# Kernel optimization log

Hardware: AMD Instinct MI355X
Metric: run time of the kernel (lower is better)

## Reference

```python
import jax, jax.numpy as jnp
import numpy as np

B, V, M, H = 256, 128, 256, 1024
TIMING_DIM = 10          # ceil(log2(max_timesteps=1024))
DECAY_ALPHA = 0.99
IN_DIM = (V + TIMING_DIM + 1 + 1) * M  # 35840


def setup_inputs() -> dict:
    key = jax.random.key(0)
    ks = jax.random.split(key, 12)
    x = jax.random.uniform(ks[0], (B, V), dtype=jnp.float32)
    memory = jax.random.uniform(ks[1], (B, M, V), dtype=jnp.float32)
    memory_timings = jax.random.randint(ks[2], (B, M), 0, 1000).astype(jnp.int64)
    memory_surprise = jax.random.uniform(ks[3], (B, M), dtype=jnp.float32)
    last_prediction = jax.random.uniform(ks[4], (B, V), dtype=jnp.float32)
    s1 = 1.0 / np.sqrt(IN_DIM)
    s2 = 1.0 / np.sqrt(H)
    W1 = jax.random.uniform(ks[5], (IN_DIM, H), dtype=jnp.float32, minval=-s1, maxval=s1)
    b1 = jnp.zeros((H,), jnp.float32)
    Wg = jax.random.uniform(ks[6], (IN_DIM, H), dtype=jnp.float32, minval=-s1, maxval=s1)
    bg = jnp.zeros((H,), jnp.float32)
    W2 = jax.random.uniform(ks[7], (H, V), dtype=jnp.float32, minval=-s2, maxval=s2)
    b2 = jnp.zeros((V,), jnp.float32)
    return {"x": x, "memory": memory, "memory_timings": memory_timings,
            "memory_surprise": memory_surprise, "last_prediction": last_prediction,
            "W1": W1, "b1": b1, "Wg": Wg, "bg": bg, "W2": W2, "b2": b2}


def _step(x, memory, memory_timings, memory_surprise, last_prediction):
    # surprise of incoming token under last prediction
    surprise = -jnp.log(jnp.sum(x * last_prediction, axis=1) + 1e-8)  # [B]
    # age + decay
    timings = memory_timings + 1
    surp = memory_surprise * DECAY_ALPHA
    # ring-buffer roll, write newest at slot 0
    mem = jnp.roll(memory, 1, axis=1).at[:, 0, :].set(x)
    timings = jnp.roll(timings, 1, axis=1).at[:, 0].set(0)
    surp = jnp.roll(surp, 1, axis=1).at[:, 0].set(surprise)
    # sort by age ascending, gather memory/surprise
    idx = jnp.argsort(timings, axis=1)                               # [B,M]
    sorted_timings = jnp.take_along_axis(timings, idx, axis=1)       # [B,M]
    sorted_memory = jnp.take_along_axis(mem, idx[..., None], axis=1)  # [B,M,V]
    sorted_surprise = jnp.take_along_axis(surp, idx, axis=1)          # [B,M]
    # binary encode timings
    powers = 2 ** jnp.arange(TIMING_DIM, dtype=sorted_timings.dtype)
    bits = ((sorted_timings[..., None] // powers) % 2).astype(jnp.float32)  # [B,M,T]
    norm_t = sorted_timings.astype(jnp.float32) / (
        jnp.max(sorted_timings, axis=1, keepdims=True).astype(jnp.float32) + 1.0)
    pred_input = jnp.concatenate(
        [sorted_memory.reshape(B, -1), bits.reshape(B, -1),
         norm_t.reshape(B, -1), sorted_surprise.reshape(B, -1)], axis=1)  # [B, IN_DIM]
    return pred_input


def reference(x, memory, memory_timings, memory_surprise, last_prediction,
              W1, b1, Wg, bg, W2, b2):
    pred_input = _step(x, memory, memory_timings, memory_surprise, last_prediction)
    # gated dense network: h = (xW1+b1) * sigmoid(xWg+bg); logits = hW2+b2
    h = (pred_input @ W1 + b1) * jax.nn.sigmoid(pred_input @ Wg + bg)
    return h @ W2 + b2
```

## Files before the change

### kernel.cpp

```cpp
#include <hip/hip_runtime.h>
#include <stdint.h>
#include <math.h>

#define BB 256
#define VV 128
#define MM 256
#define TDIM 10
#define HH 1024
#define IN_DIM 35840
#define KSPLIT 16
#define KSLICE 2240
#define BK 32
#define NCHUNK 70

using f32x4  = __attribute__((ext_vector_type(4))) float;
using bf16x8 = __attribute__((ext_vector_type(8))) short;

__device__ __forceinline__ unsigned short f2bf(float f) {
    unsigned int u = __float_as_uint(f);
    unsigned int r = (u + 0x7FFFu + ((u >> 16) & 1u)) >> 16;
    return (unsigned short)r;
}

__device__ __forceinline__ void gload_lds16(const void* g, void* l) {
    __builtin_amdgcn_global_load_lds(
        (const __attribute__((address_space(1))) unsigned int*)g,
        (__attribute__((address_space(3))) unsigned int*)l,
        16, 0, 0);
}

__global__ __launch_bounds__(512)
void k_build(const float* __restrict__ x, const float* __restrict__ memory,
             const int* __restrict__ timings, const float* __restrict__ msurp,
             const float* __restrict__ lastp, short* __restrict__ A)
{
    int b = blockIdx.x, t = threadIdx.x;
    __shared__ int t_s[MM], idx_s[MM], st_s[MM];
    __shared__ float s_surprise;

    if (t < MM) t_s[t] = (t == 0) ? 0 : timings[b*MM + t - 1] + 1;
    if (t < 64) {
        float v = x[b*VV + t] * lastp[b*VV + t]
                + x[b*VV + t + 64] * lastp[b*VV + t + 64];
        #pragma unroll
        for (int off = 32; off > 0; off >>= 1)
            v += __shfl_down(v, off, 64);
        if (t == 0) s_surprise = -logf(v + 1e-8f);
    }
    __syncthreads();

    if (t < MM) {
        int ti = t_s[t], cnt = 0;
        #pragma unroll 4
        for (int j = 0; j < MM; ++j) {
            int tj = t_s[j];
            cnt += (tj < ti) || (tj == ti && j < t);
        }
        idx_s[cnt] = t;
        st_s[cnt]  = ti;
    }
    __syncthreads();

    short* Ab = A + (size_t)b * IN_DIM;
    if (t < MM) {
        float invm = 1.f / ((float)st_s[MM-1] + 1.f);
        int st = st_s[t], src = idx_s[t];
        #pragma unroll
        for (int tt = 0; tt < TDIM; ++tt)
            Ab[32768 + t*TDIM + tt] = (short)f2bf((float)((st >> tt) & 1));
        Ab[35328 + t] = (short)f2bf((float)st * invm);
        float sv = (src == 0) ? s_surprise : msurp[b*MM + src - 1] * 0.99f;
        Ab[35584 + t] = (short)f2bf(sv);
    }

    int q4 = t >> 7, v = t & (VV-1);
    float xv = x[b*VV + v];
    #pragma unroll 8
    for (int p = q4; p < MM; p += 4) {
        int src = idx_s[p];
        int row = (src == 0) ? 0 : src - 1;
        float mv = memory[((size_t)b*MM + row)*VV + v];
        float val = (src == 0) ? xv : mv;
        Ab[p*VV + v] = (short)f2bf(val);
    }
}

__global__ __launch_bounds__(512, 4)
void k_gemm(const short* __restrict__ A, const float* __restrict__ W1,
            const float* __restrict__ Wg, float* __restrict__ P)
{
    int ks = blockIdx.x;
    int xt = blockIdx.y;
    const float* W = (xt < 16) ? W1 : Wg;
    int wcol0 = (xt & 15) * 64;
    int pcol0 = xt * 64;
    int k0 = ks * KSLICE;

    __shared__ bf16x8 As8[3][1024];
    __shared__ float  Wl[3][2048];

    int t = threadIdx.x;
    int l = t & 63, wv = t >> 6;
    int r = l & 15, q = l >> 4;
    int wm = wv & 3, nh = wv >> 2;

    int aoff[4];
    #pragma unroll
    for (int mt = 0; mt < 4; ++mt) {
        int R = wm*64 + mt*16 + r;
        aoff[mt] = R*4 + (q ^ ((R >> 1) & 3));
    }
    int ncol[2];
    #pragma unroll
    for (int nt = 0; nt < 2; ++nt) {
        int n = nh*32 + nt*16 + r;
        ncol[nt] = n ^ (q << 4);
    }

    f32x4 acc[4][2];
    #pragma unroll
    for (int mt = 0; mt < 4; ++mt)
        #pragma unroll
        for (int nt = 0; nt < 2; ++nt)
            acc[mt][nt] = (f32x4){0.f, 0.f, 0.f, 0.f};

    int wkk = t >> 4;
    int wnF = ((t & 15) * 4) ^ (((wkk >> 3) & 3) << 4);

#define STAGE(sbuf, cc) do {                                                  \
        int kc_ = k0 + (cc)*BK;                                               \
        {   int G_ = t;                                                       \
            int m_ = G_ >> 2;                                                 \
            int kb_ = (G_ & 3) ^ ((m_ >> 1) & 3);                             \
            gload_lds16(A + (size_t)m_*IN_DIM + kc_ + kb_*8,                  \
                        (char*)&As8[sbuf][0] + (size_t)(t & ~63)*16);         \
        }                                                                     \
        {   int G_ = t + 512;                                                 \
            int m_ = G_ >> 2;                                                 \
            int kb_ = (G_ & 3) ^ ((m_ >> 1) & 3);                             \
            gload_lds16(A + (size_t)m_*IN_DIM + kc_ + kb_*8,                  \
                        (char*)&As8[sbuf][0] + (size_t)((t & ~63) + 512)*16); \
        }                                                                     \
        gload_lds16(W + (size_t)(kc_ + wkk)*HH + wcol0 + wnF,                 \
                    (char*)&Wl[sbuf][0] + (size_t)(t & ~63)*16);              \
    } while (0)

    STAGE(0, 0);
    STAGE(1, 1);
    STAGE(2, 2);
    asm volatile("s_waitcnt vmcnt(6)" ::: "memory");
    __builtin_amdgcn_s_barrier();

    for (int c = 0; c < NCHUNK; ++c) {
        int buf = c % 3;

        bf16x8 af[4], bfr[2];
        #pragma unroll
        for (int mt = 0; mt < 4; ++mt) af[mt] = As8[buf][aoff[mt]];
        #pragma unroll
        for (int nt = 0; nt < 2; ++nt) {
            const float* wb = &Wl[buf][ncol[nt]];
            bf16x8 bb;
            #pragma unroll
            for (int j = 0; j < 8; ++j)
                bb[j] = (short)f2bf(wb[(q*8 + j)*64]);
            bfr[nt] = bb;
        }
        #pragma unroll
        for (int mt = 0; mt < 4; ++mt)
            #pragma unroll
            for (int nt = 0; nt < 2; ++nt)
                acc[mt][nt] = __builtin_amdgcn_mfma_f32_16x16x32_bf16(
                    af[mt], bfr[nt], acc[mt][nt], 0, 0, 0);

        __builtin_amdgcn_s_barrier();
        {
            int cn = (c + 3 < NCHUNK) ? c + 3 : NCHUNK - 1;
            STAGE(buf, cn);
        }
        asm volatile("s_waitcnt vmcnt(6)" ::: "memory");
        __builtin_amdgcn_s_barrier();
    }
#undef STAGE

    #pragma unroll
    for (int mt = 0; mt < 4; ++mt)
        #pragma unroll
        for (int nt = 0; nt < 2; ++nt)
            #pragma unroll
            for (int rg = 0; rg < 4; ++rg) {
                int m = wm*64 + mt*16 + q*4 + rg;
                int n = pcol0 + nh*32 + nt*16 + r;
                P[((size_t)ks*BB + m)*2048 + n] = acc[mt][nt][rg];
            }
}

__global__ __launch_bounds__(512)
void k_tail(const float* __restrict__ P, const float* __restrict__ b1,
            const float* __restrict__ bg, const float* __restrict__ W2,
            const float* __restrict__ b2, float* __restrict__ out)
{
    int b = blockIdx.x, t = threadIdx.x;
    __shared__ f32x4 part[512];
    __shared__ float hs[HH];
    __shared__ float s2[512];

    const f32x4* P4 = (const f32x4*)P;
    f32x4 s = (f32x4){0.f, 0.f, 0.f, 0.f};
    #pragma unroll
    for (int ks = 0; ks < KSPLIT; ++ks)
        s += P4[((size_t)ks*BB + b)*512 + t];
    part[t] = s;
    __syncthreads();

    if (t < 256) {
        f32x4 p1 = part[t]       + ((const f32x4*)b1)[t];
        f32x4 pg = part[t + 256] + ((const f32x4*)bg)[t];
        f32x4 o;
        #pragma unroll
        for (int j = 0; j < 4; ++j)
            o[j] = p1[j] / (1.f + expf(-pg[j]));
        ((f32x4*)hs)[t] = o;
    }
    __syncthreads();

    int v = t & 127, kh = t >> 7;
    const float* wp = W2 + (size_t)kh*256*VV + v;
    const float* hk = hs + kh*256;
    float acc = 0.f;
    #pragma unroll 8
    for (int k = 0; k < 256; ++k)
        acc += hk[k] * wp[(size_t)k*VV];
    s2[t] = acc;
    __syncthreads();
    if (t < 128)
        out[(size_t)b*VV + v] = s2[t] + s2[t+128] + s2[t+256] + s2[t+384] + b2[v];
}

extern "C" void kernel_launch(void* const* d_in, const int* in_sizes, int n_in,
                              void* d_out, int out_size, void* d_ws, size_t ws_size,
                              hipStream_t stream)
{
    const float* x    = (const float*)d_in[0];
    const float* mem  = (const float*)d_in[1];
    const int*   tim  = (const int*)d_in[2];
    const float* msur = (const float*)d_in[3];
    const float* lp   = (const float*)d_in[4];
    const float* W1   = (const float*)d_in[5];
    const float* b1   = (const float*)d_in[6];
    const float* Wg   = (const float*)d_in[7];
    const float* bg   = (const float*)d_in[8];
    const float* W2   = (const float*)d_in[9];
    const float* b2   = (const float*)d_in[10];
    float* out = (float*)d_out;

    short* A = (short*)d_ws;
    float* P = (float*)((char*)d_ws + 18350080);

    k_build <<<256, 512, 0, stream>>>(x, mem, tim, msur, lp, A);
    k_gemm  <<<dim3(KSPLIT, 32), 512, 0, stream>>>(A, W1, Wg, P);
    k_tail  <<<256, 512, 0, stream>>>(P, b1, bg, W2, b2, out);
}
```

Measured before the change: 403.0 us.

## Load A fragments directly to registers and convert W to bf16 once in LDS

The GEMM no longer stages A and fp32 W tiles into LDS with a triple buffer. Each wave now loads its own A rows straight from global memory into MFMA fragment registers, prefetched one chunk ahead. W is read into registers two chunks ahead, converted to bf16 once per element, and written into a small double-buffered swizzled LDS tile. The goal is to cut LDS footprint and traffic and remove redundant per-wave fp32-to-bf16 conversion. The cost is uncoalesced-ish direct global A loads and more register pressure, with a different 32x64 per-wave tiling.

```diff
diff --git a/kernel.cpp b/kernel.cpp
--- a/kernel.cpp
+++ b/kernel.cpp
@@ -22,13 +22,6 @@
     return (unsigned short)r;
 }
 
-__device__ __forceinline__ void gload_lds16(const void* g, void* l) {
-    __builtin_amdgcn_global_load_lds(
-        (const __attribute__((address_space(1))) unsigned int*)g,
-        (__attribute__((address_space(3))) unsigned int*)l,
-        16, 0, 0);
-}
-
 __global__ __launch_bounds__(512)
 void k_build(const float* __restrict__ x, const float* __restrict__ memory,
              const int* __restrict__ timings, const float* __restrict__ msurp,
@@ -96,101 +89,109 @@
     int pcol0 = xt * 64;
     int k0 = ks * KSLICE;
 
-    __shared__ bf16x8 As8[3][1024];
-    __shared__ float  Wl[3][2048];
+    __shared__ bf16x8 Ws8[2][256];
 
     int t = threadIdx.x;
     int l = t & 63, wv = t >> 6;
     int r = l & 15, q = l >> 4;
-    int wm = wv & 3, nh = wv >> 2;
-
-    int aoff[4];
-    #pragma unroll
-    for (int mt = 0; mt < 4; ++mt) {
-        int R = wm*64 + mt*16 + r;
-        aoff[mt] = R*4 + (q ^ ((R >> 1) & 3));
-    }
-    int ncol[2];
-    #pragma unroll
-    for (int nt = 0; nt < 2; ++nt) {
-        int n = nh*32 + nt*16 + r;
-        ncol[nt] = n ^ (q << 4);
-    }
-
-    f32x4 acc[4][2];
-    #pragma unroll
-    for (int mt = 0; mt < 4; ++mt)
-        #pragma unroll
-        for (int nt = 0; nt < 2; ++nt)
+
+    const short* arow[2];
+    #pragma unroll
+    for (int mt = 0; mt < 2; ++mt) {
+        int R = wv*32 + mt*16 + r;
+        arow[mt] = A + (size_t)R*IN_DIM + k0 + q*8;
+    }
+
+    int boff[4];
+    #pragma unroll
+    for (int nt = 0; nt < 4; ++nt) {
+        int R = nt*16 + r;
+        boff[nt] = R*4 + (q ^ ((R >> 1) & 3));
+    }
+
+    f32x4 acc[2][4];
+    #pragma unroll
+    for (int mt = 0; mt < 2; ++mt)
+        #pragma unroll
+        for (int nt = 0; nt < 4; ++nt)
             acc[mt][nt] = (f32x4){0.f, 0.f, 0.f, 0.f};
 
-    int wkk = t >> 4;
-    int wnF = ((t & 15) * 4) ^ (((wkk >> 3) & 3) << 4);
-
-#define STAGE(sbuf, cc) do {                                                  \
-        int kc_ = k0 + (cc)*BK;                                               \
-        {   int G_ = t;                                                       \
-            int m_ = G_ >> 2;                                                 \
-            int kb_ = (G_ & 3) ^ ((m_ >> 1) & 3);                             \
-            gload_lds16(A + (size_t)m_*IN_DIM + kc_ + kb_*8,                  \
-                        (char*)&As8[sbuf][0] + (size_t)(t & ~63)*16);         \
+    int wn = l;
+    int wkg = wv >> 1, whalf = wv & 1;
+    int wslot16 = (wn*4 + (wkg ^ ((wn >> 1) & 3))) * 16 + whalf * 8;
+    const float* wbase = W + (size_t)(k0 + wv*4)*HH + wcol0 + wn;
+
+#define LOADA(AF, cc) do {                                                    \
+        int ko_ = (cc)*BK;                                                    \
+        _Pragma("unroll")                                                     \
+        for (int mt_ = 0; mt_ < 2; ++mt_)                                     \
+            AF[mt_] = *(const bf16x8*)(arow[mt_] + ko_);                      \
+    } while (0)
+
+#define WLOAD(wreg, cc) do {                                                  \
+        const float* wp_ = wbase + (size_t)(cc)*BK*HH;                        \
+        _Pragma("unroll")                                                     \
+        for (int j_ = 0; j_ < 4; ++j_) wreg[j_] = wp_[(size_t)j_*HH];         \
+    } while (0)
+
+#define WCONV(wreg, wdst) do {                                                \
+        unsigned int lo_ = (unsigned int)f2bf(wreg[0])                        \
+                         | ((unsigned int)f2bf(wreg[1]) << 16);               \
+        unsigned int hi_ = (unsigned int)f2bf(wreg[2])                        \
+                         | ((unsigned int)f2bf(wreg[3]) << 16);               \
+        unsigned int* d_ = (unsigned int*)((char*)&Ws8[wdst][0] + wslot16);   \
+        d_[0] = lo_; d_[1] = hi_;                                             \
+    } while (0)
+
+    bf16x8 afA[2], afB[2];
+    float wA[4], wB[4], w0[4];
+
+    WLOAD(w0, 0);
+    LOADA(afA, 0);
+    WLOAD(wA, 1);
+    WCONV(w0, 0);
+    asm volatile("s_waitcnt lgkmcnt(0)" ::: "memory");
+    __builtin_amdgcn_s_barrier();
+
+#define CHUNK(c, AF, AFN, WCUR, WNXT) do {                                    \
+        int cA_ = ((c) + 1 < NCHUNK) ? (c) + 1 : NCHUNK - 1;                  \
+        int cW_ = ((c) + 2 < NCHUNK) ? (c) + 2 : NCHUNK - 1;                  \
+        LOADA(AFN, cA_);                                                      \
+        WLOAD(WNXT, cW_);                                                     \
+        {                                                                     \
+            bf16x8 bf_[4];                                                    \
+            _Pragma("unroll")                                                 \
+            for (int nt = 0; nt < 4; ++nt) bf_[nt] = Ws8[(c) & 1][boff[nt]];  \
+            _Pragma("unroll")                                                 \
+            for (int mt = 0; mt < 2; ++mt)                                    \
+                _Pragma("unroll")                                             \
+                for (int nt = 0; nt < 4; ++nt)                                \
+                    acc[mt][nt] = __builtin_amdgcn_mfma_f32_16x16x32_bf16(    \
+                        AF[mt], bf_[nt], acc[mt][nt], 0, 0, 0);               \
         }                                                                     \
-        {   int G_ = t + 512;                                                 \
-            int m_ = G_ >> 2;                                                 \
-            int kb_ = (G_ & 3) ^ ((m_ >> 1) & 3);                             \
-            gload_lds16(A + (size_t)m_*IN_DIM + kc_ + kb_*8,                  \
-                        (char*)&As8[sbuf][0] + (size_t)((t & ~63) + 512)*16); \
-        }                                                                     \
-        gload_lds16(W + (size_t)(kc_ + wkk)*HH + wcol0 + wnF,                 \
-                    (char*)&Wl[sbuf][0] + (size_t)(t & ~63)*16);              \
-    } while (0)
-
-    STAGE(0, 0);
-    STAGE(1, 1);
-    STAGE(2, 2);
-    asm volatile("s_waitcnt vmcnt(6)" ::: "memory");
-    __builtin_amdgcn_s_barrier();
-
-    for (int c = 0; c < NCHUNK; ++c) {
-        int buf = c % 3;
-
-        bf16x8 af[4], bfr[2];
-        #pragma unroll
-        for (int mt = 0; mt < 4; ++mt) af[mt] = As8[buf][aoff[mt]];
-        #pragma unroll
-        for (int nt = 0; nt < 2; ++nt) {
-            const float* wb = &Wl[buf][ncol[nt]];
-            bf16x8 bb;
-            #pragma unroll
-            for (int j = 0; j < 8; ++j)
-                bb[j] = (short)f2bf(wb[(q*8 + j)*64]);
-            bfr[nt] = bb;
-        }
-        #pragma unroll
-        for (int mt = 0; mt < 4; ++mt)
-            #pragma unroll
-            for (int nt = 0; nt < 2; ++nt)
-                acc[mt][nt] = __builtin_amdgcn_mfma_f32_16x16x32_bf16(
-                    af[mt], bfr[nt], acc[mt][nt], 0, 0, 0);
-
-        __builtin_amdgcn_s_barrier();
-        {
-            int cn = (c + 3 < NCHUNK) ? c + 3 : NCHUNK - 1;
-            STAGE(buf, cn);
-        }
-        asm volatile("s_waitcnt vmcnt(6)" ::: "memory");
-        __builtin_amdgcn_s_barrier();
-    }
-#undef STAGE
-
-    #pragma unroll
-    for (int mt = 0; mt < 4; ++mt)
-        #pragma unroll
-        for (int nt = 0; nt < 2; ++nt)
+        WCONV(WCUR, ((c) + 1) & 1);                                           \
+        asm volatile("s_waitcnt lgkmcnt(0)" ::: "memory");                    \
+        __builtin_amdgcn_s_barrier();                                         \
+    } while (0)
+
+    #pragma unroll 1
+    for (int c = 0; c < NCHUNK; c += 2) {
+        CHUNK(c,     afA, afB, wA, wB);
+        CHUNK(c + 1, afB, afA, wB, wA);
+    }
+#undef CHUNK
+#undef WCONV
+#undef WLOAD
+#undef LOADA
+
+    #pragma unroll
+    for (int mt = 0; mt < 2; ++mt)
+        #pragma unroll
+        for (int nt = 0; nt < 4; ++nt)
             #pragma unroll
             for (int rg = 0; rg < 4; ++rg) {
-                int m = wm*64 + mt*16 + q*4 + rg;
-                int n = pcol0 + nh*32 + nt*16 + r;
+                int m = wv*32 + mt*16 + q*4 + rg;
+                int n = pcol0 + nt*16 + r;
                 P[((size_t)ks*BB + m)*2048 + n] = acc[mt][nt][rg];
             }
 }
```

Result: slower. 416.3 us (+3.3%).
